# Performance work log

Hardware: AMD Instinct MI355X
Metric: run time of the kernel (lower is better)

The kernel has to match this reference:

```python
import jax, jax.numpy as jnp
import numpy as np

N, E, F_IN, GCH, H, HID, NOUT, NG = 5000, 15000, 300, 2048, 4, 2048, 768, 128
NEG_SLOPE = 0.2


def gat_conv(x, W, att_src, att_dst, bias, src, dst):
    # x: [N, Fin]; W: [Fin, H*C]; att_*: [H, C]; bias: [H*C]
    n = x.shape[0]
    h = (x @ W).reshape(n, H, GCH)                      # [N,H,C]
    a_src = (h * att_src).sum(-1)                       # [N,H]
    a_dst = (h * att_dst).sum(-1)                       # [N,H]
    e = jax.nn.leaky_relu(a_src[src] + a_dst[dst], NEG_SLOPE)  # [E,H]
    m = jax.ops.segment_max(e, dst, num_segments=n)     # segment softmax over dst
    e = jnp.exp(e - m[dst])
    s = jax.ops.segment_sum(e, dst, num_segments=n)
    alpha = e / (s[dst] + 1e-16)                        # [E,H]
    msg = h[src] * alpha[:, :, None]                    # [E,H,C]
    out = jax.ops.segment_sum(msg, dst, num_segments=n) # [N,H,C]
    return out.reshape(n, H * GCH) + bias


def setup_inputs() -> dict:
    key = jax.random.key(0)
    ks = jax.random.split(key, 32)
    d = {}
    d['x'] = jax.random.normal(ks[0], (N, F_IN), jnp.float32)
    d['edge_index'] = jax.random.randint(ks[1], (2, E), 0, N, jnp.int32)
    d['batch'] = jnp.sort(jax.random.randint(ks[2], (N,), 0, NG, jnp.int32))
    dims_in = [F_IN, HID, HID]
    i = 3
    for l, fin in enumerate(dims_in, 1):
        sc = 1.0 / np.sqrt(fin)
        d[f'W{l}'] = jax.random.normal(ks[i], (fin, H * GCH), jnp.float32) * sc; i += 1
        d[f'asrc{l}'] = jax.random.normal(ks[i], (H, GCH), jnp.float32) * 0.02; i += 1
        d[f'adst{l}'] = jax.random.normal(ks[i], (H, GCH), jnp.float32) * 0.02; i += 1
        d[f'bc{l}'] = jnp.zeros((H * GCH,), jnp.float32)
        d[f'Wh{l}'] = jax.random.normal(ks[i], (H * GCH, HID), jnp.float32) * (1.0 / np.sqrt(H * GCH)); i += 1
        d[f'bh{l}'] = jnp.zeros((HID,), jnp.float32)
    d['Wm1'] = jax.random.normal(ks[i], (GCH, 2048), jnp.float32) * (1.0 / np.sqrt(GCH)); i += 1
    d['bm1'] = jnp.zeros((2048,), jnp.float32)
    d['Wm2'] = jax.random.normal(ks[i], (2048, NOUT), jnp.float32) * (1.0 / np.sqrt(2048)); i += 1
    d['bm2'] = jnp.zeros((NOUT,), jnp.float32)
    d['ln_g'] = jnp.ones((NOUT,), jnp.float32)
    d['ln_b'] = jnp.zeros((NOUT,), jnp.float32)
    return d


def reference(x, edge_index, batch,
              W1, asrc1, adst1, bc1, Wh1, bh1,
              W2, asrc2, adst2, bc2, Wh2, bh2,
              W3, asrc3, adst3, bc3, Wh3, bh3,
              Wm1, bm1, Wm2, bm2, ln_g, ln_b):
    n = x.shape[0]
    # PyG GATConv adds self-loops by default
    loops = jnp.arange(n, dtype=edge_index.dtype)
    src = jnp.concatenate([edge_index[0], loops])
    dst = jnp.concatenate([edge_index[1], loops])

    h = gat_conv(x, W1, asrc1, adst1, bc1, src, dst)
    h = jax.nn.relu(h @ Wh1 + bh1)
    h = gat_conv(h, W2, asrc2, adst2, bc2, src, dst)
    h = jax.nn.relu(h @ Wh2 + bh2)
    h = gat_conv(h, W3, asrc3, adst3, bc3, src, dst)
    h = h @ Wh3 + bh3                                   # no relu after head_linear3

    # global mean pool over graphs
    sums = jax.ops.segment_sum(h, batch, num_segments=NG)
    cnt = jax.ops.segment_sum(jnp.ones((n,), h.dtype), batch, num_segments=NG)
    g = sums / jnp.maximum(cnt, 1.0)[:, None]           # [NG, 2048]

    g = jax.nn.relu(g @ Wm1 + bm1)
    g = g @ Wm2 + bm2                                   # [NG, NOUT]
    mu = g.mean(-1, keepdims=True)
    var = ((g - mu) ** 2).mean(-1, keepdims=True)
    return (g - mu) / jnp.sqrt(var + 1e-5) * ln_g + ln_b
```

## Files before the change

kernel.cpp:

```cpp
#include <hip/hip_runtime.h>

typedef unsigned short u16;
typedef __attribute__((ext_vector_type(8))) short short8;
typedef __attribute__((ext_vector_type(4))) short s16x4;
typedef __attribute__((ext_vector_type(4))) float f32x4;

__device__ inline u16 f2bf(float f){
  unsigned int u = __builtin_bit_cast(unsigned int, f);
  u += 0x7fffu + ((u >> 16) & 1u);
  return (u16)(u >> 16);
}
__device__ inline float bf2f(u16 h){
  unsigned int u = ((unsigned int)h) << 16;
  return __builtin_bit_cast(float, u);
}

typedef __attribute__((address_space(1))) const void* as1_t;
typedef __attribute__((address_space(3))) void* as3_t;
__device__ __forceinline__ void gload16(const u16* g, u16* l) {
  __builtin_amdgcn_global_load_lds((as1_t)g, (as3_t)l, 16, 0, 0);
}

#define BARRIER() asm volatile("s_barrier" ::: "memory")
#define VMCNT4()  asm volatile("s_waitcnt vmcnt(4)" ::: "memory")
#define VMCNT0()  asm volatile("s_waitcnt vmcnt(0)" ::: "memory")
#define LGKM0()   asm volatile("s_waitcnt lgkmcnt(0)" ::: "memory")

__device__ __forceinline__ void gemm_core(
    const u16* __restrict__ A, const u16* __restrict__ B, u16* __restrict__ C,
    int tile_m, int tile_n, int abase, int hoff,
    int M, int K, int lda, int ldb, int ldc, u16* lds)
{
  int tid = threadIdx.x, wave = tid >> 6, lane = tid & 63;
  int wm = wave >> 2, wn = wave & 3;
  int NT = K >> 6;

  const u16* sA[2]; const u16* sB[2];
  int dq[2];
#pragma unroll
  for (int q = 0; q < 2; ++q) {
    int row = q * 128 + (tid >> 2);
    int cg  = (tid & 3) ^ ((row >> 1) & 3);
    sA[q] = A + (size_t)(abase + row) * lda + hoff + cg * 8;
    sB[q] = B + (size_t)(tile_n + row) * ldb + hoff + cg * 8;
    dq[q] = q * 4096 + tid * 8;
  }

  int l15 = lane & 15, c4 = lane >> 4;
  int aoff[8], boff[4];
#pragma unroll
  for (int mi = 0; mi < 8; ++mi) {
    int r = wm * 128 + mi * 16 + l15;
    aoff[mi] = r * 32 + ((c4 ^ ((r >> 1) & 3)) * 8);
  }
#pragma unroll
  for (int ni = 0; ni < 4; ++ni) {
    int r = wn * 64 + ni * 16 + l15;
    boff[ni] = r * 32 + ((c4 ^ ((r >> 1) & 3)) * 8);
  }

  f32x4 acc[8][4];
#pragma unroll
  for (int mi = 0; mi < 8; ++mi)
#pragma unroll
    for (int ni = 0; ni < 4; ++ni) { f32x4 z = {0.f,0.f,0.f,0.f}; acc[mi][ni] = z; }

#define DSRA(fa, mb, base) \
  fa[0] = *reinterpret_cast<const short8*>(&lds[(base) + aoff[(mb)+0]]); \
  fa[1] = *reinterpret_cast<const short8*>(&lds[(base) + aoff[(mb)+1]]); \
  fa[2] = *reinterpret_cast<const short8*>(&lds[(base) + aoff[(mb)+2]]); \
  fa[3] = *reinterpret_cast<const short8*>(&lds[(base) + aoff[(mb)+3]]);
#define DSRB(fb, base) \
  fb[0] = *reinterpret_cast<const short8*>(&lds[(base) + boff[0]]); \
  fb[1] = *reinterpret_cast<const short8*>(&lds[(base) + boff[1]]); \
  fb[2] = *reinterpret_cast<const short8*>(&lds[(base) + boff[2]]); \
  fb[3] = *reinterpret_cast<const short8*>(&lds[(base) + boff[3]]);
#define MM16(mb, fa, fb) \
  _Pragma("unroll") for (int mi = 0; mi < 4; ++mi) \
  _Pragma("unroll") for (int ni = 0; ni < 4; ++ni) \
    acc[(mb)+mi][ni] = __builtin_amdgcn_mfma_f32_16x16x32_bf16(fa[mi], fb[ni], acc[(mb)+mi][ni], 0, 0, 0);
#define PH_SYNC() BARRIER(); LGKM0(); __builtin_amdgcn_sched_barrier(0)
#define PRIO1() __builtin_amdgcn_s_setprio(1)
#define PRIO0() __builtin_amdgcn_s_setprio(0)

#pragma unroll
  for (int q = 0; q < 2; ++q) {
    gload16(sA[q],      &lds[0     + dq[q]]);
    gload16(sB[q],      &lds[16384 + dq[q]]);
    gload16(sA[q] + 32, &lds[8192  + dq[q]]);
    gload16(sB[q] + 32, &lds[24576 + dq[q]]);
  }
  VMCNT0();
  BARRIER();

  for (int t = 0; t < NT; ++t) {
    int cb = (t & 1) * 32768;
    int nb = cb ^ 32768;
    bool st = (t + 1) < NT;
    int ke = (t + 1) * 64;
    short8 fa[4], fb0[4], fb1[4];
    DSRA(fa, 0, cb + 0);
    DSRB(fb0, cb + 16384);
    if (st) { gload16(sA[0] + ke, &lds[nb + dq[0]]);
              gload16(sA[1] + ke, &lds[nb + dq[1]]); }
    PH_SYNC(); PRIO1(); MM16(0, fa, fb0); PRIO0();
    BARRIER();
    DSRA(fa, 4, cb + 0);
    if (st) { gload16(sB[0] + ke, &lds[nb + 16384 + dq[0]]);
              gload16(sB[1] + ke, &lds[nb + 16384 + dq[1]]); }
    PH_SYNC(); PRIO1(); MM16(4, fa, fb0); PRIO0();
    if (st) { VMCNT4(); } else { VMCNT0(); }
    BARRIER();
    DSRA(fa, 0, cb + 8192);
    DSRB(fb1, cb + 24576);
    if (st) { gload16(sA[0] + ke + 32, &lds[nb + 8192 + dq[0]]);
              gload16(sA[1] + ke + 32, &lds[nb + 8192 + dq[1]]); }
    PH_SYNC(); PRIO1(); MM16(0, fa, fb1); PRIO0();
    BARRIER();
    DSRA(fa, 4, cb + 8192);
    if (st) { gload16(sB[0] + ke + 32, &lds[nb + 24576 + dq[0]]);
              gload16(sB[1] + ke + 32, &lds[nb + 24576 + dq[1]]); }
    PH_SYNC(); PRIO1(); MM16(4, fa, fb1); PRIO0();
    if (st) { VMCNT4(); }
    BARRIER();
  }

  int rq = (lane >> 4) * 4;
#pragma unroll
  for (int mi = 0; mi < 8; ++mi)
#pragma unroll
    for (int ni = 0; ni < 4; ++ni) {
      int col = tile_n + wn * 64 + ni * 16 + l15;
#pragma unroll
      for (int j = 0; j < 4; ++j) {
        int row = tile_m + wm * 128 + mi * 16 + rq + j;
        if (row < M) C[(size_t)row * ldc + col] = f2bf(acc[mi][ni][j]);
      }
    }
#undef DSRA
#undef DSRB
#undef MM16
#undef PH_SYNC
#undef PRIO1
#undef PRIO0
}

__global__ __launch_bounds__(512, 2) void gemm8p(
    const u16* __restrict__ A, const u16* __restrict__ B, u16* __restrict__ C,
    int M, int N, int K, int lda, int ldb, int ldc, int headed)
{
  __shared__ alignas(16) u16 lds[65536];
  int tile_m = blockIdx.y * 256, tile_n = blockIdx.x * 256;
  int hoff  = headed ? ((tile_m >> 11) << 11) : 0;
  int abase = headed ? (tile_m & 2047) : tile_m;
  gemm_core(A, B, C, tile_m, tile_n, abase, hoff, M, K, lda, ldb, ldc, lds);
}

__global__ __launch_bounds__(512, 2) void gemm8p_u2(
    const u16* A0, const u16* B0, u16* C0, int N0,
    const u16* A1, const u16* B1, u16* C1, int N1, int s1)
{
  __shared__ alignas(16) u16 lds[65536];
  int flat = blockIdx.x;
  int j = flat >= s1;
  const u16* A = j ? A1 : A0;
  const u16* B = j ? B1 : B0;
  u16*       C = j ? C1 : C0;
  int N = j ? N1 : N0;
  int lbx = flat - (j ? s1 : 0);
  int ntile = N >> 8;
  int tile_n = (lbx % ntile) * 256;
  int tile_m = (lbx / ntile) * 256;
  gemm_core(A, B, C, tile_m, tile_n, tile_m & 2047, (tile_m >> 11) << 11,
            8192, 2048, 8192, 8192, N, lds);
}

__global__ __launch_bounds__(256) void prep_w(
    const float* __restrict__ W, u16* __restrict__ Wb,
    const float* __restrict__ asrc, const float* __restrict__ adst,
    float* __restrict__ wsd, int Fin, int Fp)
{
  int f = blockIdx.x;
  int w = threadIdx.x >> 6, lane = threadIdx.x & 63;
  if (f >= Fin) {
    s16x4 z = {0,0,0,0};
#pragma unroll
    for (int i = 0; i < 8; ++i)
      *reinterpret_cast<s16x4*>(Wb + (size_t)f * 8192 + w * 2048 + lane * 4 + i * 256) = z;
    if (lane == 0) { wsd[w * Fp + f] = 0.f; wsd[(4 + w) * Fp + f] = 0.f; }
    return;
  }
  const float* wr = W + (size_t)f * 8192 + w * 2048;
  const float* as = asrc + w * 2048;
  const float* ad = adst + w * 2048;
  u16* wb = Wb + (size_t)f * 8192 + w * 2048;
  float ss = 0.f, dd = 0.f;
#pragma unroll
  for (int i = 0; i < 8; ++i) {
    int c = lane * 4 + i * 256;
    f32x4 wv = *reinterpret_cast<const f32x4*>(wr + c);
    f32x4 av = *reinterpret_cast<const f32x4*>(as + c);
    f32x4 dv = *reinterpret_cast<const f32x4*>(ad + c);
    s16x4 ov;
#pragma unroll
    for (int j = 0; j < 4; ++j) {
      ss += wv[j] * av[j]; dd += wv[j] * dv[j];
      ov[j] = (short)f2bf(wv[j]);
    }
    *reinterpret_cast<s16x4*>(wb + c) = ov;
  }
  for (int off = 32; off; off >>= 1) {
    ss += __shfl_down(ss, off);
    dd += __shfl_down(dd, off);
  }
  if (lane == 0) { wsd[w * Fp + f] = ss; wsd[(4 + w) * Fp + f] = dd; }
}

__global__ __launch_bounds__(256) void transpose_bias(
    const float* __restrict__ Wh, u16* __restrict__ Wht,
    const float* __restrict__ bc, float* __restrict__ bhp)
{
  __shared__ float tile[32][33];
  int k0 = blockIdx.x * 32, n0 = blockIdx.y * 32;
  int tx = threadIdx.x & 31, ty = threadIdx.x >> 5;
#pragma unroll
  for (int i = 0; i < 4; ++i)
    tile[ty + i * 8][tx] = Wh[(size_t)(k0 + ty + i * 8) * 2048 + n0 + tx];
  __syncthreads();
#pragma unroll
  for (int i = 0; i < 4; ++i)
    Wht[(size_t)(n0 + ty + i * 8) * 8192 + k0 + tx] = f2bf(tile[tx][ty + i * 8]);
  if (threadIdx.x < 32) {
    float p = 0.f;
#pragma unroll
    for (int kk = 0; kk < 32; ++kk) p += bc[k0 + kk] * tile[kk][threadIdx.x];
    atomicAdd(&bhp[n0 + threadIdx.x], p);
  }
}

__global__ void init_bhp(const float* b0, const float* b1, const float* b2,
                         float* bhp){
  int i = blockIdx.x * 256 + threadIdx.x;
  int l = blockIdx.y;
  if (i < 2048) {
    const float* s = (l == 0) ? b0 : (l == 1 ? b1 : b2);
    bhp[l * 2048 + i] = s[i];
  }
}

__global__ __launch_bounds__(256) void transpose_cast(
    const float* __restrict__ W, u16* __restrict__ Wt, int K, int N, int Kpad)
{
  __shared__ float tile[32][33];
  int k0 = blockIdx.x * 32, n0 = blockIdx.y * 32;
  int tx = threadIdx.x & 31, ty = threadIdx.x >> 5;
#pragma unroll
  for (int i = 0; i < 4; ++i) {
    int k = k0 + ty + i * 8;
    float v = 0.f;
    if (k < K && (n0 + tx) < N) v = W[(size_t)k * N + n0 + tx];
    tile[ty + i * 8][tx] = v;
  }
  __syncthreads();
#pragma unroll
  for (int i = 0; i < 4; ++i) {
    int nn = n0 + ty + i * 8;
    if (nn < N) Wt[(size_t)nn * Kpad + k0 + tx] = f2bf(tile[tx][ty + i * 8]);
  }
}

__global__ void cast_pad(const float* __restrict__ x, u16* __restrict__ xb,
                         int R, int C, int Cp)
{
  int i = blockIdx.x * 256 + threadIdx.x;
  if (i >= R * Cp) return;
  int r = i / Cp, c = i % Cp;
  xb[i] = f2bf(c < C ? x[(size_t)r * C + c] : 0.f);
}

__global__ __launch_bounds__(256) void a_score(
    const u16* __restrict__ xb, const float* __restrict__ wsd,
    float* __restrict__ a_s, float* __restrict__ a_d, int Fp)
{
  int n = blockIdx.x, tid = threadIdx.x, lane = tid & 63, w = tid >> 6;
  float s[4] = {0.f,0.f,0.f,0.f}, d[4] = {0.f,0.f,0.f,0.f};
  int f = tid * 8;
  if (f < Fp) {
    short8 v = *reinterpret_cast<const short8*>(xb + (size_t)n * Fp + f);
#pragma unroll
    for (int j = 0; j < 8; ++j) {
      float xv = bf2f((u16)v[j]);
#pragma unroll
      for (int h = 0; h < 4; ++h) {
        s[h] += xv * wsd[h * Fp + f + j];
        d[h] += xv * wsd[(4 + h) * Fp + f + j];
      }
    }
  }
  __shared__ float red[4][8];
#pragma unroll
  for (int h = 0; h < 4; ++h) {
    for (int off = 32; off; off >>= 1) {
      s[h] += __shfl_down(s[h], off);
      d[h] += __shfl_down(d[h], off);
    }
  }
  if (lane == 0) {
#pragma unroll
    for (int h = 0; h < 4; ++h) { red[w][h] = s[h]; red[w][4 + h] = d[h]; }
  }
  __syncthreads();
  if (tid < 8) {
    float t = red[0][tid] + red[1][tid] + red[2][tid] + red[3][tid];
    if (tid < 4) a_s[n * 4 + tid] = t;
    else         a_d[n * 4 + tid - 4] = t;
  }
}

__global__ void zero_int(int* p, int n){ int i = blockIdx.x*256+threadIdx.x; if (i < n) p[i] = 0; }

__global__ void count_deg(const int* __restrict__ ei, int E, int Nn, int* __restrict__ deg){
  int e = blockIdx.x*256+threadIdx.x; if (e >= E + Nn) return;
  int d = (e < E) ? ei[E + e] : (e - E);
  atomicAdd(&deg[d], 1);
}

__global__ void scan_deg(const int* __restrict__ deg, int* __restrict__ row_st,
                         int* __restrict__ cursor, int Nn){
  __shared__ int partial[256];
  int tid = threadIdx.x;
  int chunk = (Nn + 255) / 256;
  int start = tid * chunk;
  int sum = 0;
  for (int i = 0; i < chunk; ++i) { int idx = start + i; if (idx < Nn) sum += deg[idx]; }
  partial[tid] = sum;
  __syncthreads();
  if (tid == 0) { int acc = 0; for (int i = 0; i < 256; ++i) { int t = partial[i]; partial[i] = acc; acc += t; } }
  __syncthreads();
  int acc = partial[tid];
  for (int i = 0; i < chunk; ++i) {
    int idx = start + i;
    if (idx < Nn) { row_st[idx] = acc; cursor[idx] = acc; acc += deg[idx]; }
  }
  if (tid == 255) row_st[Nn] = acc;
}

__global__ void scatter_edges(const int* __restrict__ ei, int E, int Nn,
                              int* __restrict__ cursor, int* __restrict__ srcs){
  int e = blockIdx.x*256+threadIdx.x; if (e >= E + Nn) return;
  int s = (e < E) ? ei[e]     : (e - E);
  int d = (e < E) ? ei[E + e] : (e - E);
  int pos = atomicAdd(&cursor[d], 1);
  srcs[pos] = s;
}

__global__ void edge_softmax(const int* __restrict__ row_st, const int* __restrict__ srcs,
                             const float* __restrict__ a_s, const float* __restrict__ a_d,
                             float* __restrict__ alpha, int Nn){
  int t = blockIdx.x*256+threadIdx.x;
  if (t >= Nn * 4) return;
  int n = t >> 2, hh = t & 3;
  int b = row_st[n], e = row_st[n + 1];
  float ad = a_d[n * 4 + hh];
  float m = -1e30f;
  for (int p = b; p < e; ++p) {
    float x = a_s[srcs[p] * 4 + hh] + ad;
    x = x > 0.f ? x : 0.2f * x;
    alpha[p * 4 + hh] = x;
    m = fmaxf(m, x);
  }
  float ssum = 0.f;
  for (int p = b; p < e; ++p) {
    float ex = expf(alpha[p * 4 + hh] - m);
    alpha[p * 4 + hh] = ex;
    ssum += ex;
  }
  float inv = 1.f / (ssum + 1e-16f);
  for (int p = b; p < e; ++p) alpha[p * 4 + hh] *= inv;
}

__global__ __launch_bounds__(256) void aggregate2(
    const u16* __restrict__ z, const float* __restrict__ alpha,
    const int* __restrict__ row_st, const int* __restrict__ srcs,
    const float* __restrict__ bhp, u16* __restrict__ out, int relu,
    const float* __restrict__ wsd_next, float* __restrict__ psum)
{
  int n = blockIdx.x, half = blockIdx.y, tid = threadIdx.x;
  int c = half * 1024 + tid * 4;
  float acc[4] = {0.f, 0.f, 0.f, 0.f};
  int b = row_st[n], e = row_st[n + 1];

  int s0 = srcs[b];
  const u16* zr = z + (size_t)s0 * 8192 + c;
  s16x4 cv0 = *reinterpret_cast<const s16x4*>(zr);
  s16x4 cv1 = *reinterpret_cast<const s16x4*>(zr + 2048);
  s16x4 cv2 = *reinterpret_cast<const s16x4*>(zr + 4096);
  s16x4 cv3 = *reinterpret_cast<const s16x4*>(zr + 6144);
  float ca0 = alpha[b * 4 + 0], ca1 = alpha[b * 4 + 1];
  float ca2 = alpha[b * 4 + 2], ca3 = alpha[b * 4 + 3];
  s16x4 nv0, nv1, nv2, nv3;
  float na0 = 0.f, na1 = 0.f, na2 = 0.f, na3 = 0.f;
  if (b + 1 < e) {
    int s1 = srcs[b + 1];
    const u16* zr1 = z + (size_t)s1 * 8192 + c;
    nv0 = *reinterpret_cast<const s16x4*>(zr1);
    nv1 = *reinterpret_cast<const s16x4*>(zr1 + 2048);
    nv2 = *reinterpret_cast<const s16x4*>(zr1 + 4096);
    nv3 = *reinterpret_cast<const s16x4*>(zr1 + 6144);
    na0 = alpha[(b + 1) * 4 + 0]; na1 = alpha[(b + 1) * 4 + 1];
    na2 = alpha[(b + 1) * 4 + 2]; na3 = alpha[(b + 1) * 4 + 3];
  }

  for (int p = b; p < e; ++p) {
    s16x4 w0 = cv0, w1 = cv1, w2 = cv2, w3 = cv3;
    float b0 = ca0, b1 = ca1, b2 = ca2, b3 = ca3;
    cv0 = nv0; cv1 = nv1; cv2 = nv2; cv3 = nv3;
    ca0 = na0; ca1 = na1; ca2 = na2; ca3 = na3;
    if (p + 2 < e) {
      int s2 = srcs[p + 2];
      const u16* zr2 = z + (size_t)s2 * 8192 + c;
      nv0 = *reinterpret_cast<const s16x4*>(zr2);
      nv1 = *reinterpret_cast<const s16x4*>(zr2 + 2048);
      nv2 = *reinterpret_cast<const s16x4*>(zr2 + 4096);
      nv3 = *reinterpret_cast<const s16x4*>(zr2 + 6144);
      na0 = alpha[(p + 2) * 4 + 0]; na1 = alpha[(p + 2) * 4 + 1];
      na2 = alpha[(p + 2) * 4 + 2]; na3 = alpha[(p + 2) * 4 + 3];
    }
#pragma unroll
    for (int q = 0; q < 4; ++q)
      acc[q] += b0 * bf2f((u16)w0[q]) + b1 * bf2f((u16)w1[q])
              + b2 * bf2f((u16)w2[q]) + b3 * bf2f((u16)w3[q]);
  }

  float sv[4] = {0.f,0.f,0.f,0.f}, dv[4] = {0.f,0.f,0.f,0.f};
  s16x4 ov;
#pragma unroll
  for (int q = 0; q < 4; ++q) {
    float v = acc[q] + bhp[c + q];
    if (relu) v = fmaxf(v, 0.f);
    ov[q] = (short)f2bf(v);
    if (wsd_next) {
#pragma unroll
      for (int h = 0; h < 4; ++h) {
        sv[h] += v * wsd_next[h * 2048 + c + q];
        dv[h] += v * wsd_next[(4 + h) * 2048 + c + q];
      }
    }
  }
  *reinterpret_cast<s16x4*>(out + (size_t)n * 2048 + c) = ov;
  if (wsd_next) {
    int lane = tid & 63, w = tid >> 6;
    __shared__ float red[4][8];
#pragma unroll
    for (int h = 0; h < 4; ++h) {
      for (int off = 32; off; off >>= 1) {
        sv[h] += __shfl_down(sv[h], off);
        dv[h] += __shfl_down(dv[h], off);
      }
    }
    if (lane == 0) {
#pragma unroll
      for (int h = 0; h < 4; ++h) { red[w][h] = sv[h]; red[w][4 + h] = dv[h]; }
    }
    __syncthreads();
    if (tid < 8) {
      float t = red[0][tid] + red[1][tid] + red[2][tid] + red[3][tid];
      psum[(size_t)n * 16 + half * 8 + tid] = t;
    }
  }
}

__global__ void combine_scores(const float* __restrict__ psum,
                               float* __restrict__ a_s, float* __restrict__ a_d,
                               int Nn){
  int i = blockIdx.x * 256 + threadIdx.x;
  if (i >= Nn * 4) return;
  int n = i >> 2, h = i & 3;
  a_s[i] = psum[(size_t)n * 16 + h]     + psum[(size_t)n * 16 + 8 + h];
  a_d[i] = psum[(size_t)n * 16 + 4 + h] + psum[(size_t)n * 16 + 12 + h];
}

__global__ __launch_bounds__(256) void pool_mean(
    const u16* __restrict__ hf, const int* __restrict__ batch,
    u16* __restrict__ g, int Nn)
{
  int gid = blockIdx.x, tid = threadIdx.x;
  int s1, s2;
  { int l = 0, h = Nn; while (l < h) { int m = (l + h) >> 1; if (batch[m] < gid) l = m + 1; else h = m; } s1 = l; }
  { int l = 0, h = Nn; while (l < h) { int m = (l + h) >> 1; if (batch[m] < gid + 1) l = m + 1; else h = m; } s2 = l; }
  float inv = 1.f / fmaxf((float)(s2 - s1), 1.f);
  float acc[8];
#pragma unroll
  for (int q = 0; q < 8; ++q) acc[q] = 0.f;
  for (int r = s1; r < s2; ++r) {
    short8 v = *reinterpret_cast<const short8*>(hf + (size_t)r * 2048 + tid * 8);
#pragma unroll
    for (int q = 0; q < 8; ++q) acc[q] += bf2f((u16)v[q]);
  }
  short8 ov;
#pragma unroll
  for (int q = 0; q < 8; ++q) ov[q] = (short)f2bf(acc[q] * inv);
  *reinterpret_cast<short8*>(g + (size_t)gid * 2048 + tid * 8) = ov;
}

__global__ __launch_bounds__(256) void gemm_bt(
    const u16* __restrict__ A, const u16* __restrict__ B,
    float* __restrict__ Cf, u16* __restrict__ Cb,
    const float* __restrict__ bias, int M, int N, int K, int relu)
{
  __shared__ alignas(16) u16 As[128 * 32];
  __shared__ alignas(16) u16 Bs[128 * 32];
  int tid = threadIdx.x;
  int wave = tid >> 6, lane = tid & 63;
  int wr = wave >> 1, wc = wave & 1;
  int tile_m = blockIdx.y * 128, tile_n = blockIdx.x * 128;

  int sr = wave * 16 + (lane >> 2);
  int sc = (lane & 3) * 8;
  const u16* gA0 = A + (size_t)(tile_m + sr) * K + sc;
  const u16* gA1 = A + (size_t)(tile_m + 64 + sr) * K + sc;
  const u16* gB0 = B + (size_t)(tile_n + sr) * K + sc;
  const u16* gB1 = B + (size_t)(tile_n + 64 + sr) * K + sc;
  u16* lA0 = &As[wave * 512];
  u16* lA1 = &As[2048 + wave * 512];
  u16* lB0 = &Bs[wave * 512];
  u16* lB1 = &Bs[2048 + wave * 512];

  f32x4 acc[4][4];
#pragma unroll
  for (int mi = 0; mi < 4; ++mi)
#pragma unroll
    for (int ni = 0; ni < 4; ++ni) { f32x4 z = {0.f,0.f,0.f,0.f}; acc[mi][ni] = z; }

  int lrow = lane & 15, lk = (lane >> 4) * 8;

  for (int k0 = 0; k0 < K; k0 += 32) {
    gload16(gA0 + k0, lA0);
    gload16(gA1 + k0, lA1);
    gload16(gB0 + k0, lB0);
    gload16(gB1 + k0, lB1);
    __syncthreads();
    short8 af[4], bfr[4];
#pragma unroll
    for (int mi = 0; mi < 4; ++mi)
      af[mi] = *reinterpret_cast<const short8*>(&As[(wr * 64 + mi * 16 + lrow) * 32 + lk]);
#pragma unroll
    for (int ni = 0; ni < 4; ++ni)
      bfr[ni] = *reinterpret_cast<const short8*>(&Bs[(wc * 64 + ni * 16 + lrow) * 32 + lk]);
#pragma unroll
    for (int mi = 0; mi < 4; ++mi)
#pragma unroll
      for (int ni = 0; ni < 4; ++ni)
        acc[mi][ni] = __builtin_amdgcn_mfma_f32_16x16x32_bf16(af[mi], bfr[ni], acc[mi][ni], 0, 0, 0);
    __syncthreads();
  }

  int rquad = (lane >> 4) * 4;
#pragma unroll
  for (int mi = 0; mi < 4; ++mi)
#pragma unroll
    for (int ni = 0; ni < 4; ++ni) {
      int col = tile_n + wc * 64 + ni * 16 + lrow;
      float bv = bias ? bias[col] : 0.f;
#pragma unroll
      for (int j = 0; j < 4; ++j) {
        int row = tile_m + wr * 64 + mi * 16 + rquad + j;
        if (row < M) {
          float v = acc[mi][ni][j] + bv;
          if (relu) v = fmaxf(v, 0.f);
          if (Cb) Cb[(size_t)row * N + col] = f2bf(v);
          else    Cf[(size_t)row * N + col] = v;
        }
      }
    }
}

__global__ __launch_bounds__(256) void layernorm_768(
    const float* __restrict__ x, const float* __restrict__ gam,
    const float* __restrict__ bet, float* __restrict__ out)
{
  int row = blockIdx.x, tid = threadIdx.x, lane = tid & 63, w = tid >> 6;
  __shared__ float sh[8];
  float v0 = x[row * 768 + tid];
  float v1 = x[row * 768 + 256 + tid];
  float v2 = x[row * 768 + 512 + tid];
  float s = v0 + v1 + v2;
  for (int off = 32; off; off >>= 1) s += __shfl_down(s, off);
  if (lane == 0) sh[w] = s;
  __syncthreads();
  if (tid == 0) sh[4] = (sh[0] + sh[1] + sh[2] + sh[3]) / 768.f;
  __syncthreads();
  float mu = sh[4];
  float d0 = v0 - mu, d1 = v1 - mu, d2 = v2 - mu;
  float q = d0 * d0 + d1 * d1 + d2 * d2;
  for (int off = 32; off; off >>= 1) q += __shfl_down(q, off);
  if (lane == 0) sh[w] = q;
  __syncthreads();
  if (tid == 0) sh[5] = rsqrtf((sh[0] + sh[1] + sh[2] + sh[3]) / 768.f + 1e-5f);
  __syncthreads();
  float rstd = sh[5];
  out[row * 768 + tid]       = d0 * rstd * gam[tid]       + bet[tid];
  out[row * 768 + 256 + tid] = d1 * rstd * gam[256 + tid] + bet[256 + tid];
  out[row * 768 + 512 + tid] = d2 * rstd * gam[512 + tid] + bet[512 + tid];
}

extern "C" void kernel_launch(void* const* d_in, const int* in_sizes, int n_in,
                              void* d_out, int out_size, void* d_ws, size_t ws_size,
                              hipStream_t stream)
{
  const float* x     = (const float*)d_in[0];
  const int*   ei    = (const int*)d_in[1];
  const int*   batch = (const int*)d_in[2];
  const float* W[3]   = {(const float*)d_in[3], (const float*)d_in[9],  (const float*)d_in[15]};
  const float* asr[3] = {(const float*)d_in[4], (const float*)d_in[10], (const float*)d_in[16]};
  const float* ads[3] = {(const float*)d_in[5], (const float*)d_in[11], (const float*)d_in[17]};
  const float* bc[3]  = {(const float*)d_in[6], (const float*)d_in[12], (const float*)d_in[18]};
  const float* Wh[3]  = {(const float*)d_in[7], (const float*)d_in[13], (const float*)d_in[19]};
  const float* bh[3]  = {(const float*)d_in[8], (const float*)d_in[14], (const float*)d_in[20]};
  const float* Wm1 = (const float*)d_in[21];
  const float* bm1 = (const float*)d_in[22];
  const float* Wm2 = (const float*)d_in[23];
  const float* bm2 = (const float*)d_in[24];
  const float* lng = (const float*)d_in[25];
  const float* lnb = (const float*)d_in[26];
  float* out = (float*)d_out;

  int Nn = in_sizes[2];
  int E  = in_sizes[1] / 2;
  int ET = E + Nn;

  char* base = (char*)d_ws;
  size_t off = 0;
  auto alloc = [&](size_t b) -> char* { char* p = base + off; off = (off + b + 255) & ~(size_t)255; return p; };
  u16*  act   = (u16*)alloc((size_t)5120 * 2048 * 2);
  u16*  Wb0d  = (u16*)alloc((size_t)512  * 8192 * 2);
  u16*  Wht0d = (u16*)alloc((size_t)2048 * 8192 * 2);
  u16*  Ut0   = (u16*)alloc((size_t)8192 * 512  * 2);
  u16*  Ut1   = (u16*)alloc((size_t)8192 * 2048 * 2);
  u16*  Ut2   = (u16*)alloc((size_t)8192 * 2048 * 2);
  u16*  zb    = (u16*)alloc((size_t)5120 * 8192 * 2);
  u16*  xb0   = (u16*)alloc((size_t)5120 * 512 * 2);
  float* wsd  = (float*)alloc((size_t)3 * 8 * 2048 * 4);
  float* bhp  = (float*)alloc((size_t)3 * 2048 * 4);
  float* a_s  = (float*)alloc((size_t)Nn * 4 * 4);
  float* a_d  = (float*)alloc((size_t)Nn * 4 * 4);
  float* psum = (float*)alloc((size_t)Nn * 16 * 4);
  float* alpha= (float*)alloc((size_t)ET * 4 * 4);
  int*  deg   = (int*)alloc((size_t)(Nn + 1) * 4);
  int*  rowst = (int*)alloc((size_t)(Nn + 1) * 4);
  int*  cursor= (int*)alloc((size_t)(Nn + 1) * 4);
  int*  srcs  = (int*)alloc((size_t)ET * 4);
  u16*  g     = (u16*)alloc((size_t)128 * 2048 * 2);
  u16*  g2    = (u16*)alloc((size_t)128 * 2048 * 2);
  float* preln= (float*)alloc((size_t)128 * 768 * 4);

  u16* Wb_sh  = zb;
  u16* Wht_sh = zb + (size_t)2048 * 8192;

  zero_int<<<(Nn + 255) / 256, 256, 0, stream>>>(deg, Nn);
  count_deg<<<(ET + 255) / 256, 256, 0, stream>>>(ei, E, Nn, deg);
  scan_deg<<<1, 256, 0, stream>>>(deg, rowst, cursor, Nn);
  scatter_edges<<<(ET + 255) / 256, 256, 0, stream>>>(ei, E, Nn, cursor, srcs);
  cast_pad<<<(Nn * 512 + 255) / 256, 256, 0, stream>>>(x, xb0, Nn, 300, 512);

  init_bhp<<<dim3(8, 3), 256, 0, stream>>>(bh[0], bh[1], bh[2], bhp);
  prep_w<<<512, 256, 0, stream>>>(W[0], Wb0d, asr[0], ads[0], wsd, 300, 512);
  transpose_bias<<<dim3(256, 64), 256, 0, stream>>>(Wh[0], Wht0d, bc[0], bhp);
  prep_w<<<2048, 256, 0, stream>>>(W[1], Wb_sh, asr[1], ads[1], wsd + 16384, 2048, 2048);
  transpose_bias<<<dim3(256, 64), 256, 0, stream>>>(Wh[1], Wht_sh, bc[1], bhp + 2048);
  gemm8p_u2<<<320, 512, 0, stream>>>(Wht0d, Wb0d, Ut0, 512,
                                     Wht_sh, Wb_sh, Ut1, 2048, 64);
  prep_w<<<2048, 256, 0, stream>>>(W[2], Wb_sh, asr[2], ads[2], wsd + 32768, 2048, 2048);
  transpose_bias<<<dim3(256, 64), 256, 0, stream>>>(Wh[2], Wht_sh, bc[2], bhp + 4096);
  gemm8p<<<dim3(8, 32), 512, 0, stream>>>(Wht_sh, Wb_sh, Ut2, 8192, 2048, 2048, 8192, 8192, 2048, 1);

  a_score<<<Nn, 256, 0, stream>>>(xb0, wsd, a_s, a_d, 512);

  const u16* actcur = xb0;
  u16* Ut[3] = {Ut0, Ut1, Ut2};
  for (int l = 0; l < 3; ++l) {
    int Fp = (l == 0) ? 512 : 2048;
    edge_softmax<<<(Nn * 4 + 255) / 256, 256, 0, stream>>>(rowst, srcs, a_s, a_d, alpha, Nn);
    gemm8p<<<dim3(32, 20), 512, 0, stream>>>(actcur, Ut[l], zb, Nn, 8192, Fp, Fp, Fp, 8192, 0);
    aggregate2<<<dim3(Nn, 2), 256, 0, stream>>>(zb, alpha, rowst, srcs, bhp + l * 2048, act,
                                                (l < 2) ? 1 : 0,
                                                (l < 2) ? (wsd + (l + 1) * 16384) : nullptr,
                                                psum);
    if (l < 2)
      combine_scores<<<(Nn * 4 + 255) / 256, 256, 0, stream>>>(psum, a_s, a_d, Nn);
    actcur = act;
  }

  pool_mean<<<128, 256, 0, stream>>>(act, batch, g, Nn);
  u16* Mt1 = zb;
  u16* Mt2 = zb + (size_t)2048 * 2048;
  transpose_cast<<<dim3(64, 64), 256, 0, stream>>>(Wm1, Mt1, 2048, 2048, 2048);
  gemm_bt<<<dim3(16, 1), 256, 0, stream>>>(g, Mt1, nullptr, g2, bm1, 128, 2048, 2048, 1);
  transpose_cast<<<dim3(64, 24), 256, 0, stream>>>(Wm2, Mt2, 2048, 768, 2048);
  gemm_bt<<<dim3(6, 1), 256, 0, stream>>>(g2, Mt2, preln, nullptr, bm2, 128, 768, 2048, 0);
  layernorm_768<<<128, 256, 0, stream>>>(preln, lng, lnb, out);
}
```

Baseline: 1.249 ms.

## Trim layer-1 K padding, swizzle GEMM workgroups across XCDs, nontemporal output stores

For the first layer's large GEMM, K drops from the padded 512 to 320 (still a multiple of 64) while the leading dimension stays 512, so the zero-padded columns are no longer multiplied. The per-layer GEMM also remaps workgroup IDs so that neighbouring tiles land on the same XCD, aiming for better L2 reuse of A/B tiles, and writes its bf16 output with nontemporal stores to avoid polluting the cache. The risks are that nontemporal stores may slow the following aggregate kernel that reads zb, and that the swizzle assumes the grid size is divisible by 8 (640 is).

```diff
diff --git a/kernel.cpp b/kernel.cpp
--- a/kernel.cpp
+++ b/kernel.cpp
@@ -29,7 +29,7 @@
 __device__ __forceinline__ void gemm_core(
     const u16* __restrict__ A, const u16* __restrict__ B, u16* __restrict__ C,
     int tile_m, int tile_n, int abase, int hoff,
-    int M, int K, int lda, int ldb, int ldc, u16* lds)
+    int M, int K, int lda, int ldb, int ldc, int ntst, u16* lds)
 {
   int tid = threadIdx.x, wave = tid >> 6, lane = tid & 63;
   int wm = wave >> 2, wn = wave & 3;
@@ -134,7 +134,11 @@
 #pragma unroll
       for (int j = 0; j < 4; ++j) {
         int row = tile_m + wm * 128 + mi * 16 + rq + j;
-        if (row < M) C[(size_t)row * ldc + col] = f2bf(acc[mi][ni][j]);
+        if (row < M) {
+          u16 v = f2bf(acc[mi][ni][j]);
+          if (ntst) __builtin_nontemporal_store(v, &C[(size_t)row * ldc + col]);
+          else      C[(size_t)row * ldc + col] = v;
+        }
       }
     }
 #undef DSRA
@@ -147,13 +151,21 @@
 
 __global__ __launch_bounds__(512, 2) void gemm8p(
     const u16* __restrict__ A, const u16* __restrict__ B, u16* __restrict__ C,
-    int M, int N, int K, int lda, int ldb, int ldc, int headed)
+    int M, int N, int K, int lda, int ldb, int ldc, int headed, int xswz, int ntst)
 {
   __shared__ alignas(16) u16 lds[65536];
-  int tile_m = blockIdx.y * 256, tile_n = blockIdx.x * 256;
+  int gx = gridDim.x;
+  int wg = blockIdx.y * gx + blockIdx.x;
+  if (xswz) {
+    int nwg = gx * gridDim.y;
+    int q = nwg >> 3;
+    wg = (wg & 7) * q + (wg >> 3);
+  }
+  int tile_n = (wg % gx) * 256;
+  int tile_m = (wg / gx) * 256;
   int hoff  = headed ? ((tile_m >> 11) << 11) : 0;
   int abase = headed ? (tile_m & 2047) : tile_m;
-  gemm_core(A, B, C, tile_m, tile_n, abase, hoff, M, K, lda, ldb, ldc, lds);
+  gemm_core(A, B, C, tile_m, tile_n, abase, hoff, M, K, lda, ldb, ldc, ntst, lds);
 }
 
 __global__ __launch_bounds__(512, 2) void gemm8p_u2(
@@ -172,7 +184,7 @@
   int tile_n = (lbx % ntile) * 256;
   int tile_m = (lbx / ntile) * 256;
   gemm_core(A, B, C, tile_m, tile_n, tile_m & 2047, (tile_m >> 11) << 11,
-            8192, 2048, 8192, 8192, N, lds);
+            8192, 2048, 8192, 8192, N, 0, lds);
 }
 
 __global__ __launch_bounds__(256) void prep_w(
@@ -672,16 +684,17 @@
                                      Wht_sh, Wb_sh, Ut1, 2048, 64);
   prep_w<<<2048, 256, 0, stream>>>(W[2], Wb_sh, asr[2], ads[2], wsd + 32768, 2048, 2048);
   transpose_bias<<<dim3(256, 64), 256, 0, stream>>>(Wh[2], Wht_sh, bc[2], bhp + 4096);
-  gemm8p<<<dim3(8, 32), 512, 0, stream>>>(Wht_sh, Wb_sh, Ut2, 8192, 2048, 2048, 8192, 8192, 2048, 1);
+  gemm8p<<<dim3(8, 32), 512, 0, stream>>>(Wht_sh, Wb_sh, Ut2, 8192, 2048, 2048, 8192, 8192, 2048, 1, 0, 0);
 
   a_score<<<Nn, 256, 0, stream>>>(xb0, wsd, a_s, a_d, 512);
 
   const u16* actcur = xb0;
   u16* Ut[3] = {Ut0, Ut1, Ut2};
   for (int l = 0; l < 3; ++l) {
-    int Fp = (l == 0) ? 512 : 2048;
+    int Kz  = (l == 0) ? 320 : 2048;
+    int ldz = (l == 0) ? 512 : 2048;
     edge_softmax<<<(Nn * 4 + 255) / 256, 256, 0, stream>>>(rowst, srcs, a_s, a_d, alpha, Nn);
-    gemm8p<<<dim3(32, 20), 512, 0, stream>>>(actcur, Ut[l], zb, Nn, 8192, Fp, Fp, Fp, 8192, 0);
+    gemm8p<<<dim3(32, 20), 512, 0, stream>>>(actcur, Ut[l], zb, Nn, 8192, Kz, ldz, ldz, 8192, 0, 1, 1);
     aggregate2<<<dim3(Nn, 2), 256, 0, stream>>>(zb, alpha, rowst, srcs, bhp + l * 2048, act,
                                                 (l < 2) ? 1 : 0,
                                                 (l < 2) ? (wsd + (l + 1) * 16384) : nullptr,
```

New measurement: 1.238 ms. About the same (-0.9%).
